# Kernel tuning notes

Hardware: AMD Instinct MI355X
Metric: run time of the kernel (lower is better)

Reference implementation:

```python
import jax, jax.numpy as jnp
import numpy as np


def setup_inputs() -> dict:
    key = jax.random.key(0)
    ks = jax.random.split(key, 8)
    B, N, C = 4, 2048, 1024
    H, hd, lr, R = 16, 64, 20, 200  # R = low_rank * rank_multi
    s = lambda k, shape, fan: jax.random.normal(k, shape, jnp.float32) / np.sqrt(fan)
    return {
        'x': jax.random.normal(ks[0], (B, N, C), jnp.float32),
        'qk_w': s(ks[1], (2 * C, C), C),
        'proj_w': s(ks[2], (C, C), C),
        'proj_b': jnp.zeros((C,), jnp.float32),
        'we': s(ks[3], (H, R, lr), R),
        'wr': s(ks[4], (H, R, lr), R),
        'cw_w': s(ks[5], (hd, 2 * lr), 2 * lr),
        'cw_b': jnp.zeros((hd,), jnp.float32),
    }


def _l2norm(v, eps=1e-12):
    # matches F.normalize(p=2, dim=-1): x / max(||x||, eps)
    n = jnp.sqrt(jnp.sum(v * v, axis=-1, keepdims=True))
    return v / jnp.maximum(n, eps)


def reference(x, qk_w, proj_w, proj_b, we, wr, cw_w, cw_b):
    B, N, C = x.shape
    H, R, lr = we.shape  # heads, subsample len, low_rank
    hd = C // H
    # qk projection -> q,k: [B,H,N,hd]
    qk = (x @ qk_w.T).reshape(B, N, 2, H, hd).transpose(2, 0, 3, 1, 4)
    q, k = qk[0], qk[1]
    # gen_weights: subsample N positions (embed_len > low_rank*rank_multi branch)
    idx = np.linspace(0, N - 1, R).astype(np.int64)  # static, trunc like torch
    xh = x.transpose(0, 2, 1).reshape(B, H, hd, N)[:, :, :, idx]  # [B,H,hd,R]
    we_b = jnp.einsum('bhdr,hre->bhde', xh, we)  # [B,H,hd,lr]
    wr_b = jnp.einsum('bhdr,hre->bhde', xh, wr)
    # feature map + low-rank scores
    q = _l2norm(q)
    k = _l2norm(k)
    escore = jnp.einsum('bhnd,bhde->bhne', q, we_b)  # [B,H,N,lr]
    rscore = jnp.einsum('bhnd,bhde->bhne', k, wr_b)
    score = jnp.concatenate([escore, rscore], axis=-1)  # [B,H,N,2lr]
    attn = score @ cw_w.T + cw_b  # [B,H,N,hd]
    attn = attn.transpose(0, 2, 1, 3).reshape(B, N, C)
    out = attn @ proj_w.T + proj_b  # dropout is identity at eval
    return out
```

## Files before the change

### kernel.cpp

```cpp
#include <hip/hip_runtime.h>
#include <hip/hip_bf16.h>

constexpr int B_  = 4;
constexpr int N_  = 2048;
constexpr int C_  = 1024;
constexpr int H_  = 16;
constexpr int HD  = 64;
constexpr int LR  = 20;
constexpr int RS  = 200;
constexpr int RP  = 224;

typedef __attribute__((ext_vector_type(8))) short bf16x8;
typedef __attribute__((ext_vector_type(4))) float f32x4;

__device__ __forceinline__ float b2f_raw(unsigned short u) {
    union { unsigned int i; float f; } v;
    v.i = ((unsigned int)u) << 16;
    return v.f;
}
__device__ __forceinline__ unsigned short f2b(float f) {
    __hip_bfloat16 h = __float2bfloat16(f);
    return *(unsigned short*)&h;
}
template <bool BF>
__device__ __forceinline__ float ldg(const void* p, size_t i) {
    if constexpr (BF) return b2f_raw(((const unsigned short*)p)[i]);
    else              return ((const float*)p)[i];
}

__device__ __forceinline__ void async_load16(const unsigned short* g, unsigned short* l) {
    __builtin_amdgcn_global_load_lds(
        (const __attribute__((address_space(1))) unsigned int*)(const void*)g,
        (__attribute__((address_space(3))) unsigned int*)(void*)l,
        16, 0, 0);
}

__global__ __launch_bounds__(256)
void detect_kernel(const unsigned int* __restrict__ x, int* __restrict__ flag) {
    const int t = threadIdx.x;
    int cnt = 0;
    for (int i = t; i < 1024; i += 256) {
        const unsigned int w = x[i];
        const unsigned int e = (w >> 7) & 0xFFu;
        cnt += (e >= 103u && e <= 140u) ? 1 : 0;
    }
    __shared__ int s[256];
    s[t] = cnt;
    __syncthreads();
    for (int off = 128; off > 0; off >>= 1) {
        if (t < off) s[t] += s[t + off];
        __syncthreads();
    }
    if (t == 0) *flag = (s[0] > 512) ? 1 : 0;
}

struct CvtArgs {
    const void* src[5];
    unsigned short* dst[5];
    int size[5];
};

template <bool BF>
__device__ void wec_body(const void* __restrict__ we_raw,
                         const void* __restrict__ wr_raw,
                         const void* __restrict__ cw_raw,
                         unsigned short* __restrict__ wect,
                         unsigned short* __restrict__ wrct) {
    const int o = blockIdx.x * 256 + threadIdx.x;
    if (o >= H_ * HD * RP) return;
    const int r    = o % RP;
    const int dout = (o / RP) % HD;
    const int h    = o / (RP * HD);
    float sq = 0.f, sk = 0.f;
    if (r < RS) {
        #pragma unroll
        for (int e = 0; e < LR; ++e) {
            const float cq = ldg<BF>(cw_raw, dout * 2 * LR + e);
            const float ck = ldg<BF>(cw_raw, dout * 2 * LR + LR + e);
            sq += ldg<BF>(we_raw, ((size_t)h * RS + r) * LR + e) * cq;
            sk += ldg<BF>(wr_raw, ((size_t)h * RS + r) * LR + e) * ck;
        }
    }
    wect[o] = f2b(sq);
    wrct[o] = f2b(sk);
}

template <bool BF>
__device__ void gather_body(const void* __restrict__ x_raw,
                            unsigned short* __restrict__ xh) {
    const int bh = blockIdx.x;
    if (bh >= B_ * H_) return;
    const int b = bh >> 4;
    const int h = bh & 15;
    for (int o = threadIdx.x; o < HD * RP; o += 256) {
        const int din = o & 63;
        const int r   = o >> 6;
        unsigned short v = 0;
        if (r < RS) {
            const int ir = (r * (N_ - 1)) / (RS - 1);
            const size_t idx = ((size_t)b * N_ + ir) * C_ + h * HD + din;
            if constexpr (BF) v = ((const unsigned short*)x_raw)[idx];
            else              v = f2b(((const float*)x_raw)[idx]);
        }
        xh[(size_t)bh * HD * RP + (size_t)din * RP + r] = v;
    }
}

__global__ __launch_bounds__(256)
void fused_prep_kernel(const int* __restrict__ flag, CvtArgs args,
                       const void* __restrict__ we_raw,
                       const void* __restrict__ wr_raw,
                       const void* __restrict__ cw_raw,
                       unsigned short* __restrict__ wect,
                       unsigned short* __restrict__ wrct,
                       unsigned short* __restrict__ xh) {
    const bool isbf = (*flag != 0);
    const int y = blockIdx.y;
    if (y < 5) {
        const int n4 = args.size[y] >> 2;
        const int stride = gridDim.x * blockDim.x;
        for (int i = blockIdx.x * blockDim.x + threadIdx.x; i < n4; i += stride) {
            ushort4 o;
            if (isbf) {
                o = ((const ushort4*)args.src[y])[i];
            } else {
                const float4 v = ((const float4*)args.src[y])[i];
                o.x = f2b(v.x); o.y = f2b(v.y); o.z = f2b(v.z); o.w = f2b(v.w);
            }
            ((ushort4*)args.dst[y])[i] = o;
        }
    } else if (y == 5) {
        if (isbf) wec_body<true>(we_raw, wr_raw, cw_raw, wect, wrct);
        else      wec_body<false>(we_raw, wr_raw, cw_raw, wect, wrct);
    } else {
        if (isbf) gather_body<true>(args.src[0], xh);
        else      gather_body<false>(args.src[0], xh);
    }
}

__global__ __launch_bounds__(64)
void collapse_kernel(const unsigned short* __restrict__ xh,
                     const unsigned short* __restrict__ wect,
                     const unsigned short* __restrict__ wrct,
                     unsigned short* __restrict__ we2t,
                     unsigned short* __restrict__ wr2t) {
    const int blk = blockIdx.x;
    const int bh  = blk >> 2;
    const int qk  = (blk >> 1) & 1;
    const int dh  = blk & 1;
    const int h   = bh & 15;
    const int lane = threadIdx.x;
    const int lq = lane >> 4;
    const int lm = lane & 15;

    const unsigned short* wsrc = (qk ? wrct : wect) + (size_t)h * HD * RP;
    const unsigned short* xsrc = xh + (size_t)bh * HD * RP;
    unsigned short* dst = (qk ? wr2t : we2t) + (size_t)bh * HD * HD;

    f32x4 acc[2][4];
    #pragma unroll
    for (int i = 0; i < 2; ++i)
        #pragma unroll
        for (int j = 0; j < 4; ++j) acc[i][j] = 0.f;

    for (int ks = 0; ks < RP / 32; ++ks) {
        bf16x8 a[2], bfr[4];
        #pragma unroll
        for (int rt = 0; rt < 2; ++rt)
            a[rt] = *(const bf16x8*)&wsrc[(size_t)(dh * 32 + rt * 16 + lm) * RP + ks * 32 + lq * 8];
        #pragma unroll
        for (int j = 0; j < 4; ++j)
            bfr[j] = *(const bf16x8*)&xsrc[(size_t)(j * 16 + lm) * RP + ks * 32 + lq * 8];
        #pragma unroll
        for (int rt = 0; rt < 2; ++rt)
            #pragma unroll
            for (int j = 0; j < 4; ++j)
                acc[rt][j] = __builtin_amdgcn_mfma_f32_16x16x32_bf16(
                    a[rt], bfr[j], acc[rt][j], 0, 0, 0);
    }

    #pragma unroll
    for (int rt = 0; rt < 2; ++rt)
        #pragma unroll
        for (int j = 0; j < 4; ++j)
            #pragma unroll
            for (int r = 0; r < 4; ++r) {
                const int dout = dh * 32 + rt * 16 + lq * 4 + r;
                const int din  = j * 16 + lm;
                dst[dout * HD + din] = f2b(acc[rt][j][r]);
            }
}

__global__ __launch_bounds__(256, 4)
void gemm1_score_kernel(const unsigned short* __restrict__ xb,
                        const unsigned short* __restrict__ qkwb,
                        const unsigned short* __restrict__ we2t,
                        const unsigned short* __restrict__ wr2t,
                        const unsigned short* __restrict__ cwbb,
                        unsigned short* __restrict__ attn) {
    constexpr int QS = 72;
    __shared__ __align__(16) unsigned short pool[2 * 128 * QS];
    unsigned short* As0 = pool;
    unsigned short* As1 = pool + 4096;
    unsigned short* Bs0 = pool + 8192;
    unsigned short* Bs1 = pool + 12288;
    unsigned short* qn  = pool;
    unsigned short* kn  = pool + 128 * QS;

    const int t    = threadIdx.x;
    const int wave = t >> 6;
    const int lane = t & 63;
    const int h    = blockIdx.x;
    const int m0   = blockIdx.y * 128;
    const int K    = C_;

    const int srow = lane >> 2;
    const int scol = ((lane & 3) ^ ((srow >> 1) & 3)) * 8;
    const unsigned short* ga0 = xb + (size_t)(m0 + wave * 16 + srow) * K + scol;
    const unsigned short* ga1 = ga0 + (size_t)64 * K;
    const unsigned short* gb0 = qkwb + (size_t)(h * HD + wave * 16 + srow) * K + scol;
    const unsigned short* gb1 = gb0 + (size_t)C_ * K;

    const int wr = (wave >> 1) * 64;
    const int wc = (wave & 1) * 64;
    const int lq = lane >> 4;
    const int lm = lane & 15;
    const int cx = (lq ^ ((lm >> 1) & 3)) * 8;

    f32x4 acc[4][4];
    #pragma unroll
    for (int i = 0; i < 4; ++i)
        #pragma unroll
        for (int j = 0; j < 4; ++j) acc[i][j] = 0.f;

    auto stage = [&](unsigned short* dA, unsigned short* dB) {
        async_load16(ga0, dA + wave * 512);
        async_load16(ga1, dA + (wave + 4) * 512);
        async_load16(gb0, dB + wave * 512);
        async_load16(gb1, dB + (wave + 4) * 512);
        ga0 += 32; ga1 += 32; gb0 += 32; gb1 += 32;
    };
    auto compute = [&](const unsigned short* As, const unsigned short* Bs) {
        bf16x8 af[4], bfr[4];
        #pragma unroll
        for (int i = 0; i < 4; ++i)
            af[i] = *(const bf16x8*)&As[(wr + i * 16 + lm) * 32 + cx];
        #pragma unroll
        for (int j = 0; j < 4; ++j)
            bfr[j] = *(const bf16x8*)&Bs[(wc + j * 16 + lm) * 32 + cx];
        #pragma unroll
        for (int i = 0; i < 4; ++i)
            #pragma unroll
            for (int j = 0; j < 4; ++j)
                acc[i][j] = __builtin_amdgcn_mfma_f32_16x16x32_bf16(
                    af[i], bfr[j], acc[i][j], 0, 0, 0);
    };

    constexpr int NT = C_ / 32;
    stage(As0, Bs0);
    __syncthreads();
    for (int kt = 0; kt < NT - 2; kt += 2) {
        stage(As1, Bs1);
        compute(As0, Bs0);
        __syncthreads();
        stage(As0, Bs0);
        compute(As1, Bs1);
        __syncthreads();
    }
    stage(As1, Bs1);
    compute(As0, Bs0);
    __syncthreads();
    compute(As1, Bs1);
    __syncthreads();

    unsigned short* dst = (wc == 0) ? qn : kn;
    #pragma unroll
    for (int i = 0; i < 4; ++i) {
        float inv[4];
        #pragma unroll
        for (int r = 0; r < 4; ++r) {
            float s = 0.f;
            #pragma unroll
            for (int j = 0; j < 4; ++j) s += acc[i][j][r] * acc[i][j][r];
            s += __shfl_xor(s, 1, 64);
            s += __shfl_xor(s, 2, 64);
            s += __shfl_xor(s, 4, 64);
            s += __shfl_xor(s, 8, 64);
            inv[r] = 1.f / fmaxf(sqrtf(s), 1e-12f);
        }
        #pragma unroll
        for (int j = 0; j < 4; ++j)
            #pragma unroll
            for (int r = 0; r < 4; ++r) {
                const int row = wr + i * 16 + lq * 4 + r;
                dst[row * QS + j * 16 + lm] = f2b(acc[i][j][r] * inv[r]);
            }
    }
    __syncthreads();

    const int b  = blockIdx.y >> 4;
    const int bh = b * H_ + h;
    const unsigned short* wq = we2t + (size_t)bh * HD * HD;
    const unsigned short* wk = wr2t + (size_t)bh * HD * HD;

    bf16x8 bq[2][4], bk[2][4];
    #pragma unroll
    for (int t2 = 0; t2 < 2; ++t2)
        #pragma unroll
        for (int j = 0; j < 4; ++j) {
            const int dout = j * 16 + lm;
            bq[t2][j] = *(const bf16x8*)&wq[dout * HD + t2 * 32 + lq * 8];
            bk[t2][j] = *(const bf16x8*)&wk[dout * HD + t2 * 32 + lq * 8];
        }

    f32x4 accS[2][4];
    #pragma unroll
    for (int rt = 0; rt < 2; ++rt)
        #pragma unroll
        for (int j = 0; j < 4; ++j) accS[rt][j] = 0.f;

    #pragma unroll
    for (int rt = 0; rt < 2; ++rt) {
        const int lr = wave * 32 + rt * 16 + lm;
        bf16x8 aq0 = *(const bf16x8*)&qn[lr * QS + lq * 8];
        bf16x8 aq1 = *(const bf16x8*)&qn[lr * QS + 32 + lq * 8];
        bf16x8 ak0 = *(const bf16x8*)&kn[lr * QS + lq * 8];
        bf16x8 ak1 = *(const bf16x8*)&kn[lr * QS + 32 + lq * 8];
        #pragma unroll
        for (int j = 0; j < 4; ++j) {
            accS[rt][j] = __builtin_amdgcn_mfma_f32_16x16x32_bf16(aq0, bq[0][j], accS[rt][j], 0, 0, 0);
            accS[rt][j] = __builtin_amdgcn_mfma_f32_16x16x32_bf16(aq1, bq[1][j], accS[rt][j], 0, 0, 0);
            accS[rt][j] = __builtin_amdgcn_mfma_f32_16x16x32_bf16(ak0, bk[0][j], accS[rt][j], 0, 0, 0);
            accS[rt][j] = __builtin_amdgcn_mfma_f32_16x16x32_bf16(ak1, bk[1][j], accS[rt][j], 0, 0, 0);
        }
    }

    #pragma unroll
    for (int rt = 0; rt < 2; ++rt)
        #pragma unroll
        for (int j = 0; j < 4; ++j) {
            const int dout = j * 16 + lm;
            const float bv = b2f_raw(cwbb[dout]);
            #pragma unroll
            for (int r = 0; r < 4; ++r) {
                const int row = m0 + wave * 32 + rt * 16 + lq * 4 + r;
                attn[(size_t)row * C_ + h * HD + dout] = f2b(accS[rt][j][r] + bv);
            }
        }
}

template <bool OBF>
__device__ void mfma_gemm_body32(const unsigned short* __restrict__ A,
                                 const unsigned short* __restrict__ W,
                                 const unsigned short* __restrict__ bias,
                                 void* __restrict__ out,
                                 int M, int N, int K) {
    __shared__ __align__(16) unsigned short As0[4096], As1[4096];
    __shared__ __align__(16) unsigned short Bs0[4096], Bs1[4096];

    const int t    = threadIdx.x;
    const int wave = t >> 6;
    const int lane = t & 63;
    const int m0   = blockIdx.y * 128;
    const int n0   = blockIdx.x * 128;

    const int srow = lane >> 2;
    const int scol = ((lane & 3) ^ ((srow >> 1) & 3)) * 8;
    const unsigned short* ga0 = A + (size_t)(m0 + wave * 16 + srow) * K + scol;
    const unsigned short* ga1 = ga0 + (size_t)64 * K;
    const unsigned short* gb0 = W + (size_t)(n0 + wave * 16 + srow) * K + scol;
    const unsigned short* gb1 = gb0 + (size_t)64 * K;

    const int wr = (wave >> 1) * 64;
    const int wc = (wave & 1) * 64;
    const int lq = lane >> 4;
    const int lm = lane & 15;
    const int cx = (lq ^ ((lm >> 1) & 3)) * 8;

    f32x4 acc[4][4];
    #pragma unroll
    for (int i = 0; i < 4; ++i)
        #pragma unroll
        for (int j = 0; j < 4; ++j) acc[i][j] = 0.f;

    auto stage = [&](unsigned short* dA, unsigned short* dB) {
        async_load16(ga0, dA + wave * 512);
        async_load16(ga1, dA + (wave + 4) * 512);
        async_load16(gb0, dB + wave * 512);
        async_load16(gb1, dB + (wave + 4) * 512);
        ga0 += 32; ga1 += 32; gb0 += 32; gb1 += 32;
    };
    auto compute = [&](const unsigned short* As, const unsigned short* Bs) {
        bf16x8 af[4], bfr[4];
        #pragma unroll
        for (int i = 0; i < 4; ++i)
            af[i] = *(const bf16x8*)&As[(wr + i * 16 + lm) * 32 + cx];
        #pragma unroll
        for (int j = 0; j < 4; ++j)
            bfr[j] = *(const bf16x8*)&Bs[(wc + j * 16 + lm) * 32 + cx];
        #pragma unroll
        for (int i = 0; i < 4; ++i)
            #pragma unroll
            for (int j = 0; j < 4; ++j)
                acc[i][j] = __builtin_amdgcn_mfma_f32_16x16x32_bf16(
                    af[i], bfr[j], acc[i][j], 0, 0, 0);
    };

    const int NT = K / 32;
    stage(As0, Bs0);
    __syncthreads();
    for (int kt = 0; kt < NT - 2; kt += 2) {
        stage(As1, Bs1);
        compute(As0, Bs0);
        __syncthreads();
        stage(As0, Bs0);
        compute(As1, Bs1);
        __syncthreads();
    }
    stage(As1, Bs1);
    compute(As0, Bs0);
    __syncthreads();
    compute(As1, Bs1);

    #pragma unroll
    for (int i = 0; i < 4; ++i) {
        #pragma unroll
        for (int j = 0; j < 4; ++j) {
            const int col = n0 + wc + j * 16 + lm;
            const float bv = b2f_raw(bias[col]);
            #pragma unroll
            for (int r = 0; r < 4; ++r) {
                const int row = m0 + wr + i * 16 + lq * 4 + r;
                const float v = acc[i][j][r] + bv;
                if constexpr (OBF)
                    ((__hip_bfloat16*)out)[(size_t)row * N + col] = __float2bfloat16(v);
                else
                    ((float*)out)[(size_t)row * N + col] = v;
            }
        }
    }
}

__global__ __launch_bounds__(256, 4)
void gemm2_kernel(const int* __restrict__ flag,
                  const unsigned short* __restrict__ attn,
                  const unsigned short* __restrict__ pwb,
                  const unsigned short* __restrict__ pbb,
                  void* __restrict__ out) {
    if (*flag) mfma_gemm_body32<true>(attn, pwb, pbb, out, B_ * N_, C_, C_);
    else       mfma_gemm_body32<false>(attn, pwb, pbb, out, B_ * N_, C_, C_);
}

extern "C" void kernel_launch(void* const* d_in, const int* in_sizes, int n_in,
                              void* d_out, int out_size, void* d_ws, size_t ws_size,
                              hipStream_t stream) {
    (void)in_sizes; (void)n_in; (void)out_size; (void)ws_size;

    char* ws = (char*)d_ws;
    size_t off = 0;
    auto alloc = [&](size_t bytes) {
        char* p = ws + off;
        off += (bytes + 255) & ~(size_t)255;
        return p;
    };

    int* flag = (int*)alloc(16);
    unsigned short* xb    = (unsigned short*)alloc((size_t)B_ * N_ * C_ * 2);
    unsigned short* qkwb  = (unsigned short*)alloc((size_t)2 * C_ * C_ * 2);
    unsigned short* pwb   = (unsigned short*)alloc((size_t)C_ * C_ * 2);
    unsigned short* pbb   = (unsigned short*)alloc((size_t)C_ * 2);
    unsigned short* cwbb  = (unsigned short*)alloc((size_t)HD * 2);
    unsigned short* attn  = (unsigned short*)alloc((size_t)B_ * N_ * C_ * 2);
    unsigned short* we2t  = (unsigned short*)alloc((size_t)B_ * H_ * HD * HD * 2);
    unsigned short* wr2t  = (unsigned short*)alloc((size_t)B_ * H_ * HD * HD * 2);
    unsigned short* wect  = (unsigned short*)alloc((size_t)H_ * HD * RP * 2);
    unsigned short* wrct  = (unsigned short*)alloc((size_t)H_ * HD * RP * 2);
    unsigned short* xh    = (unsigned short*)alloc((size_t)B_ * H_ * HD * RP * 2);

    const int M = B_ * N_;

    detect_kernel<<<1, 256, 0, stream>>>((const unsigned int*)d_in[0], flag);

    CvtArgs ca;
    ca.src[0] = d_in[0]; ca.dst[0] = xb;   ca.size[0] = B_ * N_ * C_;
    ca.src[1] = d_in[1]; ca.dst[1] = qkwb; ca.size[1] = 2 * C_ * C_;
    ca.src[2] = d_in[2]; ca.dst[2] = pwb;  ca.size[2] = C_ * C_;
    ca.src[3] = d_in[3]; ca.dst[3] = pbb;  ca.size[3] = C_;
    ca.src[4] = d_in[7]; ca.dst[4] = cwbb; ca.size[4] = HD;
    fused_prep_kernel<<<dim3(2048, 7), 256, 0, stream>>>(
        flag, ca, d_in[4], d_in[5], d_in[6], wect, wrct, xh);

    collapse_kernel<<<B_ * H_ * 4, 64, 0, stream>>>(xh, wect, wrct, we2t, wr2t);

    gemm1_score_kernel<<<dim3(H_, M / 128), 256, 0, stream>>>(
        xb, qkwb, we2t, wr2t, cwbb, attn);

    gemm2_kernel<<<dim3(C_ / 128, M / 128), 256, 0, stream>>>(
        flag, attn, pwb, pbb, d_out);
}
```

Baseline: 209.1 us.

## Triple-buffer async LDS staging with vmcnt-based waits in both GEMMs

Both MFMA GEMM main loops move from double-buffered staging with full __syncthreads to a three-buffer ring. Each step uses an inline s_waitcnt vmcnt(4) plus s_barrier, so two tiles of global-to-LDS loads can be in flight while one tile is computed. The aim is to hide global load latency that the old double buffer exposed at every barrier. The cost is 50% more LDS per block, so launch bounds drop to 3 and 2 blocks per CU, which lowers occupancy. Correctness relies on each stage issuing exactly four vector memory ops per thread.

```diff
diff --git a/kernel.cpp b/kernel.cpp
--- a/kernel.cpp
+++ b/kernel.cpp
@@ -12,6 +12,8 @@
 
 typedef __attribute__((ext_vector_type(8))) short bf16x8;
 typedef __attribute__((ext_vector_type(4))) float f32x4;
+
+#define WAITBAR(N) asm volatile("s_waitcnt vmcnt(" #N ") lgkmcnt(0)\n\ts_barrier" ::: "memory")
 
 __device__ __forceinline__ float b2f_raw(unsigned short u) {
     union { unsigned int i; float f; } v;
@@ -191,7 +193,7 @@
             }
 }
 
-__global__ __launch_bounds__(256, 4)
+__global__ __launch_bounds__(256, 3)
 void gemm1_score_kernel(const unsigned short* __restrict__ xb,
                         const unsigned short* __restrict__ qkwb,
                         const unsigned short* __restrict__ we2t,
@@ -199,13 +201,15 @@
                         const unsigned short* __restrict__ cwbb,
                         unsigned short* __restrict__ attn) {
     constexpr int QS = 72;
-    __shared__ __align__(16) unsigned short pool[2 * 128 * QS];
-    unsigned short* As0 = pool;
-    unsigned short* As1 = pool + 4096;
-    unsigned short* Bs0 = pool + 8192;
-    unsigned short* Bs1 = pool + 12288;
-    unsigned short* qn  = pool;
-    unsigned short* kn  = pool + 128 * QS;
+    __shared__ __align__(16) unsigned short pool[24576];
+    unsigned short* A0 = pool;
+    unsigned short* A1 = pool + 4096;
+    unsigned short* A2 = pool + 8192;
+    unsigned short* B0 = pool + 12288;
+    unsigned short* B1 = pool + 16384;
+    unsigned short* B2 = pool + 20480;
+    unsigned short* qn = pool;
+    unsigned short* kn = pool + 128 * QS;
 
     const int t    = threadIdx.x;
     const int wave = t >> 6;
@@ -257,20 +261,15 @@
     };
 
     constexpr int NT = C_ / 32;
-    stage(As0, Bs0);
-    __syncthreads();
-    for (int kt = 0; kt < NT - 2; kt += 2) {
-        stage(As1, Bs1);
-        compute(As0, Bs0);
-        __syncthreads();
-        stage(As0, Bs0);
-        compute(As1, Bs1);
-        __syncthreads();
-    }
-    stage(As1, Bs1);
-    compute(As0, Bs0);
-    __syncthreads();
-    compute(As1, Bs1);
+    stage(A0, B0);
+    stage(A1, B1);
+    for (int kt = 0; kt < NT - 2; kt += 3) {
+        WAITBAR(4); stage(A2, B2); compute(A0, B0);
+        WAITBAR(4); stage(A0, B0); compute(A1, B1);
+        WAITBAR(4); stage(A1, B1); compute(A2, B2);
+    }
+    WAITBAR(4); compute(A0, B0);
+    WAITBAR(0); compute(A1, B1);
     __syncthreads();
 
     unsigned short* dst = (wc == 0) ? qn : kn;
@@ -355,8 +354,8 @@
                                  const unsigned short* __restrict__ bias,
                                  void* __restrict__ out,
                                  int M, int N, int K) {
-    __shared__ __align__(16) unsigned short As0[4096], As1[4096];
-    __shared__ __align__(16) unsigned short Bs0[4096], Bs1[4096];
+    __shared__ __align__(16) unsigned short As0[4096], As1[4096], As2[4096];
+    __shared__ __align__(16) unsigned short Bs0[4096], Bs1[4096], Bs2[4096];
 
     const int t    = threadIdx.x;
     const int wave = t >> 6;
@@ -408,19 +407,14 @@
 
     const int NT = K / 32;
     stage(As0, Bs0);
-    __syncthreads();
-    for (int kt = 0; kt < NT - 2; kt += 2) {
-        stage(As1, Bs1);
-        compute(As0, Bs0);
-        __syncthreads();
-        stage(As0, Bs0);
-        compute(As1, Bs1);
-        __syncthreads();
-    }
     stage(As1, Bs1);
-    compute(As0, Bs0);
-    __syncthreads();
-    compute(As1, Bs1);
+    for (int kt = 0; kt < NT - 2; kt += 3) {
+        WAITBAR(4); stage(As2, Bs2); compute(As0, Bs0);
+        WAITBAR(4); stage(As0, Bs0); compute(As1, Bs1);
+        WAITBAR(4); stage(As1, Bs1); compute(As2, Bs2);
+    }
+    WAITBAR(4); compute(As0, Bs0);
+    WAITBAR(0); compute(As1, Bs1);
 
     #pragma unroll
     for (int i = 0; i < 4; ++i) {
@@ -441,7 +435,7 @@
     }
 }
 
-__global__ __launch_bounds__(256, 4)
+__global__ __launch_bounds__(256, 2)
 void gemm2_kernel(const int* __restrict__ flag,
                   const unsigned short* __restrict__ attn,
                   const unsigned short* __restrict__ pwb,
```

New measurement: 213.2 us. No clear change (+2.0%).
